# Optimization experiments

Hardware: AMD Instinct MI355X
Metric: run time of the kernel (lower is better)

Reference implementation:

```python
import jax, jax.numpy as jnp
import numpy as np

T_VALUES = (2.0, 8.0, 32.0, 128.0)
EPS = 1e-05
N_BANDS = 128


def setup_inputs() -> dict:
    key = jax.random.key(0)
    k1, k2, k3, k4 = jax.random.split(key, 4)
    x = jax.random.uniform(k1, (8, N_BANDS, 8192), dtype=jnp.float32)
    # Parameters are stored in log-space, matching the torch module's init
    # (log(alpha), log(delta), log(r) broadcast to n_bands).
    log_alpha = jnp.full((N_BANDS,), np.log(0.8), dtype=jnp.float32)
    log_delta = jnp.full((N_BANDS,), np.log(10.0), dtype=jnp.float32)
    log_r = jnp.full((N_BANDS,), np.log(0.25), dtype=jnp.float32)
    return {"x": x, "log_alpha": log_alpha, "log_delta": log_delta, "log_r": log_r}


def reference(x, log_alpha, log_delta, log_r):
    # x: [B, F, N]  (batch, bands, time frames)
    t_vals = jnp.asarray(T_VALUES, dtype=x.dtype)
    # s = (sqrt(1 + 4 t^2) - 1) / (2 t^2)  -- smoothing coefficient per rate
    s_vals = (jnp.sqrt(1.0 + 4.0 * t_vals ** 2) - 1.0) / (2.0 * t_vals ** 2)

    alpha = jnp.exp(log_alpha)[:, None]  # [F, 1]
    delta = jnp.exp(log_delta)[:, None]
    r = jnp.exp(log_r)[:, None]

    xt = jnp.moveaxis(x, -1, 0)  # [N, B, F], scan over time

    def ema(s):
        # IIR recursion m[t] = s*x[t] + (1-s)*m[t-1], m[-1] = x[0].
        # This is exactly what the torch triangular-matmul formulation computes:
        # smoother[t] = s * sum_{i<=t} x[i] (1-s)^{t-i} + (1-s)^{t+1} x[0].
        def step(m, xi):
            m = s * xi + (1.0 - s) * m
            return m, m
        _, ys = jax.lax.scan(step, xt[0], xt)
        return jnp.moveaxis(ys, 0, -1)  # [B, F, N]

    smoother = jax.vmap(ema)(s_vals)  # [T, B, F, N]

    # smooth = (eps + smoother)^(-alpha), written as in the source via log1p
    smooth = jnp.exp(-alpha * (jnp.log(EPS) + jnp.log1p(smoother / EPS)))
    pcen = (x[None] * smooth + delta) ** r - delta ** r  # [T, B, F, N]
    return jnp.transpose(pcen, (1, 0, 2, 3))  # [B, T, F, N]
```

## Files before the change

### kernel.cpp

```cpp
#include <hip/hip_runtime.h>

#define NB    128
#define NT    8192
#define TPB   256
#define CHUNK 32

__device__ __forceinline__ int swz(int n) { return n ^ (((n >> 5) & 7) << 2); }

__global__ __launch_bounds__(TPB, 4) void mrpcen_kernel(
    const float* __restrict__ x,
    const float* __restrict__ log_alpha,
    const float* __restrict__ log_delta,
    const float* __restrict__ log_r,
    float* __restrict__ out)
{
    __shared__ __align__(16) float sh[NT];
    __shared__ float4 sB4[TPB];

    const int tid = threadIdx.x;
    const int bf  = blockIdx.x;
    const int b   = bf >> 7;
    const int f   = bf & (NB - 1);

    const float* xrow = x + (size_t)bf * NT;

    const float alpha  = __expf(log_alpha[f]);
    const float r      = __expf(log_r[f]);
    const float delta  = __expf(log_delta[f]);
    const float deltar = __expf(r * log_delta[f]);

    float s[4], A[4];
    const float tv[4] = {2.f, 8.f, 32.f, 128.f};
#pragma unroll
    for (int t = 0; t < 4; t++) {
        float t2 = tv[t] * tv[t];
        s[t] = (sqrtf(1.f + 4.f * t2) - 1.f) / (2.f * t2);
        float a1 = 1.f - s[t];
        float a = a1 * a1; a = a * a; a = a * a; a = a * a; a = a * a;
        A[t] = a;
    }

#pragma unroll
    for (int k = 0; k < 8; k++) {
        int n = k * 1024 + tid * 4;
        float4 v = *reinterpret_cast<const float4*>(xrow + n);
        *reinterpret_cast<float4*>(&sh[swz(n)]) = v;
    }
    __syncthreads();

    const float x0 = sh[0];

    float xc[CHUNK];
#pragma unroll
    for (int j = 0; j < 8; j++) {
        int n = tid * CHUNK + 4 * j;
        float4 v = *reinterpret_cast<const float4*>(&sh[swz(n)]);
        xc[4 * j + 0] = v.x; xc[4 * j + 1] = v.y;
        xc[4 * j + 2] = v.z; xc[4 * j + 3] = v.w;
    }

    float Bl[4] = {0.f, 0.f, 0.f, 0.f};
#pragma unroll
    for (int i = 0; i < CHUNK; i++) {
        float xi = xc[i];
#pragma unroll
        for (int t = 0; t < 4; t++)
            Bl[t] = s[t] * xi + (1.f - s[t]) * Bl[t];
    }

    sB4[tid] = make_float4(Bl[0], Bl[1], Bl[2], Bl[3]);
    float ap0 = A[0], ap1 = A[1], ap2 = A[2], ap3 = A[3];
    for (int d = 1; d < TPB; d <<= 1) {
        __syncthreads();
        float4 cur = sB4[tid];
        float4 prev = make_float4(0.f, 0.f, 0.f, 0.f);
        if (tid >= d) prev = sB4[tid - d];
        __syncthreads();
        if (tid >= d) {
            cur.x += ap0 * prev.x;
            cur.y += ap1 * prev.y;
            cur.z += ap2 * prev.z;
            cur.w += ap3 * prev.w;
            sB4[tid] = cur;
        }
        ap0 *= ap0; ap1 *= ap1; ap2 *= ap2; ap3 *= ap3;
    }
    __syncthreads();
    float4 Sp = (tid > 0) ? sB4[tid - 1] : make_float4(0.f, 0.f, 0.f, 0.f);
    const float Sprev[4] = {Sp.x, Sp.y, Sp.z, Sp.w};

    float m_in[4];
#pragma unroll
    for (int t = 0; t < 4; t++) {
        float p = 1.f, base = A[t];
        int e = tid;
#pragma unroll
        for (int bit = 0; bit < 8; bit++) {
            if (e & 1) p *= base;
            base *= base;
            e >>= 1;
        }
        m_in[t] = p * x0 + Sprev[t];
    }

    for (int t = 0; t < 4; t++) {
        const float st = s[t], a1 = 1.f - s[t];
        float m = m_in[t];
#pragma unroll
        for (int j = 0; j < 8; j++) {
            float ov[4];
#pragma unroll
            for (int q = 0; q < 4; q++) {
                float xi = xc[4 * j + q];
                m = st * xi + a1 * m;
                float smooth = __expf(-alpha * __logf(1e-5f + m));
                ov[q] = __expf(r * __logf(xi * smooth + delta)) - deltar;
            }
            float4 o = make_float4(ov[0], ov[1], ov[2], ov[3]);
            *reinterpret_cast<float4*>(&sh[swz(tid * CHUNK + 4 * j)]) = o;
        }
        __syncthreads();
        float* oplane = out + (((size_t)b * 4 + t) * NB + f) * (size_t)NT;
#pragma unroll
        for (int k = 0; k < 8; k++) {
            int n = k * 1024 + tid * 4;
            float4 v = *reinterpret_cast<const float4*>(&sh[swz(n)]);
            *reinterpret_cast<float4*>(oplane + n) = v;
        }
        __syncthreads();
    }
}

extern "C" void kernel_launch(void* const* d_in, const int* in_sizes, int n_in,
                              void* d_out, int out_size, void* d_ws, size_t ws_size,
                              hipStream_t stream) {
    const float* x         = (const float*)d_in[0];
    const float* log_alpha = (const float*)d_in[1];
    const float* log_delta = (const float*)d_in[2];
    const float* log_r     = (const float*)d_in[3];
    float* out = (float*)d_out;

    mrpcen_kernel<<<dim3(8 * NB), dim3(TPB), 0, stream>>>(
        x, log_alpha, log_delta, log_r, out);
}
```

Baseline: 187.3 us.

## Split rates across blocks and use wave-shuffle scan for EMA prefix

Launches one block per (batch, band, rate) instead of one per (batch, band), so each block computes a single smoothing rate and writes one output plane. The block-wide shared-memory Hillis-Steele scan with many barriers is replaced by a 64-lane shuffle scan plus a small cross-wave combine through four shared floats. This gives four times as many blocks and fewer barriers. In exchange, each x row is loaded from global memory four times and the chunk-local recurrence is recomputed per rate.

```diff
diff --git a/kernel.cpp b/kernel.cpp
--- a/kernel.cpp
+++ b/kernel.cpp
@@ -15,30 +15,30 @@
     float* __restrict__ out)
 {
     __shared__ __align__(16) float sh[NT];
-    __shared__ float4 sB4[TPB];
+    __shared__ float sWagg[4];
 
-    const int tid = threadIdx.x;
-    const int bf  = blockIdx.x;
-    const int b   = bf >> 7;
-    const int f   = bf & (NB - 1);
+    const int tid  = threadIdx.x;
+    const int lane = tid & 63;
+    const int wid  = tid >> 6;
 
-    const float* xrow = x + (size_t)bf * NT;
+    const int bft = blockIdx.x;
+    const int t   = bft & 3;
+    const int f   = (bft >> 2) & (NB - 1);
+    const int b   = bft >> 9;
+
+    const float* xrow = x + (size_t)(b * NB + f) * NT;
 
     const float alpha  = __expf(log_alpha[f]);
     const float r      = __expf(log_r[f]);
     const float delta  = __expf(log_delta[f]);
     const float deltar = __expf(r * log_delta[f]);
 
-    float s[4], A[4];
-    const float tv[4] = {2.f, 8.f, 32.f, 128.f};
-#pragma unroll
-    for (int t = 0; t < 4; t++) {
-        float t2 = tv[t] * tv[t];
-        s[t] = (sqrtf(1.f + 4.f * t2) - 1.f) / (2.f * t2);
-        float a1 = 1.f - s[t];
-        float a = a1 * a1; a = a * a; a = a * a; a = a * a; a = a * a;
-        A[t] = a;
-    }
+    const float tt = (float)(2 << (2 * t));
+    const float t2 = tt * tt;
+    const float s  = (sqrtf(1.f + 4.f * t2) - 1.f) / (2.f * t2);
+    const float a1 = 1.f - s;
+    float A = a1;
+    A = A * A; A = A * A; A = A * A; A = A * A; A = A * A;
 
 #pragma unroll
     for (int k = 0; k < 8; k++) {
@@ -59,75 +59,66 @@
         xc[4 * j + 2] = v.z; xc[4 * j + 3] = v.w;
     }
 
-    float Bl[4] = {0.f, 0.f, 0.f, 0.f};
+    float Bl = 0.f;
 #pragma unroll
-    for (int i = 0; i < CHUNK; i++) {
-        float xi = xc[i];
+    for (int i = 0; i < CHUNK; i++)
+        Bl = s * xc[i] + a1 * Bl;
+
+    float v = Bl;
+    float ap = A;
 #pragma unroll
-        for (int t = 0; t < 4; t++)
-            Bl[t] = s[t] * xi + (1.f - s[t]) * Bl[t];
+    for (int d = 1; d < 64; d <<= 1) {
+        float up = __shfl_up(v, d);
+        if (lane >= d) v += ap * up;
+        ap *= ap;
     }
+    const float a64 = ap;
+    if (lane == 63) sWagg[wid] = v;
+    __syncthreads();
 
-    sB4[tid] = make_float4(Bl[0], Bl[1], Bl[2], Bl[3]);
-    float ap0 = A[0], ap1 = A[1], ap2 = A[2], ap3 = A[3];
-    for (int d = 1; d < TPB; d <<= 1) {
-        __syncthreads();
-        float4 cur = sB4[tid];
-        float4 prev = make_float4(0.f, 0.f, 0.f, 0.f);
-        if (tid >= d) prev = sB4[tid - d];
-        __syncthreads();
-        if (tid >= d) {
-            cur.x += ap0 * prev.x;
-            cur.y += ap1 * prev.y;
-            cur.z += ap2 * prev.z;
-            cur.w += ap3 * prev.w;
-            sB4[tid] = cur;
+    const float W0 = sWagg[0], W1 = sWagg[1], W2 = sWagg[2];
+    float pre = 0.f;
+    if (wid >= 1) pre = W0;
+    if (wid >= 2) pre = a64 * pre + W1;
+    if (wid >= 3) pre = a64 * pre + W2;
+
+    float pl = 1.f, base = A;
+    int e = lane;
+#pragma unroll
+    for (int bit = 0; bit < 6; bit++) {
+        if (e & 1) pl *= base;
+        base *= base;
+        e >>= 1;
+    }
+    float aw = 1.f;
+    const float a128 = a64 * a64;
+    if (wid & 1) aw *= a64;
+    if (wid & 2) aw *= a128;
+
+    const float vprev = __shfl_up(v, 1);
+    float m = pl * (aw * x0 + pre) + ((lane > 0) ? vprev : 0.f);
+
+#pragma unroll
+    for (int j = 0; j < 8; j++) {
+        float ov[4];
+#pragma unroll
+        for (int q = 0; q < 4; q++) {
+            float xi = xc[4 * j + q];
+            m = s * xi + a1 * m;
+            float smooth = __expf(-alpha * __logf(1e-5f + m));
+            ov[q] = __expf(r * __logf(xi * smooth + delta)) - deltar;
         }
-        ap0 *= ap0; ap1 *= ap1; ap2 *= ap2; ap3 *= ap3;
+        *reinterpret_cast<float4*>(&sh[swz(tid * CHUNK + 4 * j)]) =
+            make_float4(ov[0], ov[1], ov[2], ov[3]);
     }
     __syncthreads();
-    float4 Sp = (tid > 0) ? sB4[tid - 1] : make_float4(0.f, 0.f, 0.f, 0.f);
-    const float Sprev[4] = {Sp.x, Sp.y, Sp.z, Sp.w};
 
-    float m_in[4];
+    float* oplane = out + (((size_t)b * 4 + t) * NB + f) * (size_t)NT;
 #pragma unroll
-    for (int t = 0; t < 4; t++) {
-        float p = 1.f, base = A[t];
-        int e = tid;
-#pragma unroll
-        for (int bit = 0; bit < 8; bit++) {
-            if (e & 1) p *= base;
-            base *= base;
-            e >>= 1;
-        }
-        m_in[t] = p * x0 + Sprev[t];
-    }
-
-    for (int t = 0; t < 4; t++) {
-        const float st = s[t], a1 = 1.f - s[t];
-        float m = m_in[t];
-#pragma unroll
-        for (int j = 0; j < 8; j++) {
-            float ov[4];
-#pragma unroll
-            for (int q = 0; q < 4; q++) {
-                float xi = xc[4 * j + q];
-                m = st * xi + a1 * m;
-                float smooth = __expf(-alpha * __logf(1e-5f + m));
-                ov[q] = __expf(r * __logf(xi * smooth + delta)) - deltar;
-            }
-            float4 o = make_float4(ov[0], ov[1], ov[2], ov[3]);
-            *reinterpret_cast<float4*>(&sh[swz(tid * CHUNK + 4 * j)]) = o;
-        }
-        __syncthreads();
-        float* oplane = out + (((size_t)b * 4 + t) * NB + f) * (size_t)NT;
-#pragma unroll
-        for (int k = 0; k < 8; k++) {
-            int n = k * 1024 + tid * 4;
-            float4 v = *reinterpret_cast<const float4*>(&sh[swz(n)]);
-            *reinterpret_cast<float4*>(oplane + n) = v;
-        }
-        __syncthreads();
+    for (int k = 0; k < 8; k++) {
+        int n = k * 1024 + tid * 4;
+        float4 o = *reinterpret_cast<const float4*>(&sh[swz(n)]);
+        *reinterpret_cast<float4*>(oplane + n) = o;
     }
 }
 
@@ -140,6 +131,6 @@
     const float* log_r     = (const float*)d_in[3];
     float* out = (float*)d_out;
 
-    mrpcen_kernel<<<dim3(8 * NB), dim3(TPB), 0, stream>>>(
+    mrpcen_kernel<<<dim3(8 * NB * 4), dim3(TPB), 0, stream>>>(
         x, log_alpha, log_delta, log_r, out);
 }
```

Result: faster. 169.0 us (-9.8%).
